# Optimization experiments

Hardware: AMD Instinct MI355X
Metric: run time of the kernel (lower is better)

Reference implementation:

```python
import jax, jax.numpy as jnp
import numpy as np

IMG = 640
STRIDES = (8, 16, 32)
A = 5            # anchors per level
NC = 80          # num classes
IOU_TH = 0.5
NEG_RATIO = 1.0


def make_priors():
    scales = [1.0, 1.5, 2.0, 2.5, 3.0]
    out = []
    for s in STRIDES:
        f = IMG // s
        ys, xs = np.meshgrid(np.arange(f), np.arange(f), indexing='ij')
        cx = ((xs + 0.5) / f).ravel()
        cy = ((ys + 0.5) / f).ravel()
        for sc in scales:  # anchor-major to match merge_features (A, h, w) order
            wh = min(sc * 4.0 * s / IMG, 1.0)
            out.append(np.stack([cx, cy, np.full_like(cx, wh), np.full_like(cx, wh)], 1))
    return np.concatenate(out, 0).astype(np.float32)  # [42000, 4] cxcywh


def merge_features(feats):
    outs = []
    for feat in feats:
        n, c, h, w = feat.shape
        f = feat.reshape(n, A, c // A, h, w).transpose(0, 1, 3, 4, 2)
        outs.append(f.reshape(n, A * h * w, c // A))
    return jnp.concatenate(outs, axis=1)  # [n, M, 85]


def box_iou_cxcywh(a, b):
    # a [T,4], b [M,4] (cx,cy,w,h) -> IoU [T,M]
    a1 = jnp.concatenate([a[:, :2] - a[:, 2:] / 2, a[:, :2] + a[:, 2:] / 2], -1)
    b1 = jnp.concatenate([b[:, :2] - b[:, 2:] / 2, b[:, :2] + b[:, 2:] / 2], -1)
    tl = jnp.maximum(a1[:, None, :2], b1[None, :, :2])
    br = jnp.minimum(a1[:, None, 2:], b1[None, :, 2:])
    wh = jnp.clip(br - tl, 0.0)
    inter = wh[..., 0] * wh[..., 1]
    area_a = a[:, 2] * a[:, 3]
    area_b = b[:, 2] * b[:, 3]
    return inter / (area_a[:, None] + area_b[None, :] - inter + 1e-9)


def build_targets(targets, priors, batch):
    ious = box_iou_cxcywh(targets[:, 2:6], priors)  # [Nt, M]
    Nt, M = ious.shape
    img_ids = targets[:, 0].astype(jnp.int32)

    def per_image(i):
        valid = img_ids == i  # [Nt]
        iv = jnp.where(valid[:, None], ious, -1.0)
        best_gt_overlap = iv.max(0)            # [M]
        best_gt_idx = iv.argmax(0)             # [M]
        best_prior_idx = iv.argmax(1)          # [Nt]
        # torch: index_fill_(1) then sequential best_gt_overlap[best_prior_idx[j]] = j
        local_j = (jnp.cumsum(valid.astype(jnp.int32)) - 1).astype(jnp.float32)
        scat_idx = jnp.where(valid, best_prior_idx, M)  # drop invalid rows
        best_gt_overlap = best_gt_overlap.at[scat_idx].set(local_j, mode='drop')
        bbox = targets[best_gt_idx, 2:6]
        clss = targets[best_gt_idx, 1] + 1.0
        clss = jnp.where(best_gt_overlap < IOU_TH, 0.0, clss)
        t_xy = (bbox[:, :2] - priors[:, :2]) / priors[:, 2:]
        t_wh = jnp.log(bbox[:, 2:] / priors[:, 2:])
        return t_xy, t_wh, clss

    return jax.vmap(per_image)(jnp.arange(batch))  # [B,M,2],[B,M,2],[B,M]


def _smooth_l1(x):
    ax = jnp.abs(x)
    return jnp.where(ax < 1.0, 0.5 * ax * ax, ax - 0.5)


def compute_loss(preds, priors, targets):
    n, m, _ = preds.shape
    t_xy, t_wh, t_cls = build_targets(targets, priors, n)
    pos = t_cls > 0
    posf = pos.astype(preds.dtype)
    num_pos = posf.sum()

    # lbox: smooth L1 on xy and wh over positives (mean over pos*2 elements each)
    den2 = jnp.maximum(num_pos * 2.0, 1.0)
    lbox = (_smooth_l1(preds[..., 0:2] - t_xy) * posf[..., None]).sum() / den2 \
         + (_smooth_l1(preds[..., 2:4] - t_wh) * posf[..., None]).sum() / den2

    # lcls: cross entropy over positives, labels = t_cls - 1
    labels = jnp.clip(t_cls.astype(jnp.int32) - 1, 0, NC - 1)
    logz = jax.nn.log_softmax(preds[..., 5:], axis=-1)
    ce = -jnp.take_along_axis(logz, labels[..., None], axis=-1)[..., 0]
    lcls = (ce * posf).sum() / jnp.maximum(num_pos, 1.0)

    # hard negative mining (no grad): double argsort rank trick
    obj = preds[..., 4]
    loss_c = jax.lax.stop_gradient(-jax.nn.log_sigmoid(obj))
    loss_c = jnp.where(pos, 0.0, loss_c)
    order = jnp.argsort(-loss_c, axis=-1)
    rank = jnp.argsort(order, axis=-1)
    num_neg = jnp.minimum(NEG_RATIO * num_pos, m - num_pos)
    neg = rank.astype(preds.dtype) < num_neg
    sel = (pos | neg).astype(preds.dtype)

    # lobj: BCE-with-logits over pos|neg
    z = posf
    bce = jnp.maximum(obj, 0.0) - obj * z + jnp.log1p(jnp.exp(-jnp.abs(obj)))
    lobj = (bce * sel).sum() / jnp.maximum(sel.sum(), 1.0)

    loss = lbox + lcls + lobj
    return jnp.stack([loss, lbox, lobj, lcls])


def setup_inputs() -> dict:
    key = jax.random.key(0)
    ks = jax.random.split(key, 6)
    feat0 = jax.random.normal(ks[0], (8, 425, 80, 80), jnp.float32)
    feat1 = jax.random.normal(ks[1], (8, 425, 40, 40), jnp.float32)
    feat2 = jax.random.normal(ks[2], (8, 425, 20, 20), jnp.float32)
    B, T = 8, 20
    img = jnp.repeat(jnp.arange(B, dtype=jnp.float32), T)
    cls = jax.random.randint(ks[3], (B * T,), 0, NC).astype(jnp.float32)
    cxcy = jax.random.uniform(ks[4], (B * T, 2), minval=0.2, maxval=0.8)
    wh = jax.random.uniform(ks[5], (B * T, 2), minval=0.05, maxval=0.3)
    targets = jnp.concatenate([img[:, None], cls[:, None], cxcy, wh], 1)
    priors = jnp.asarray(make_priors())
    return {"feat0": feat0, "feat1": feat1, "feat2": feat2,
            "targets": targets, "priors": priors}


def reference(feat0, feat1, feat2, targets, priors):
    preds = merge_features([feat0, feat1, feat2])  # [8, 42000, 85]
    return compute_loss(preds, priors, targets)    # [loss, lbox, lobj, lcls]
```

## Files before the change

### kernel.cpp

```cpp
#include <hip/hip_runtime.h>
#include <math.h>

#define MTOT 42000
#define NB 8
#define NCLS 80
#define CAP_LIST 4096
#define MAXT 256
#define NT_MAX 2048
#define GX_MAIN 165
#define NBLK_MAIN (GX_MAIN*NB)
#define NBLK_SEL 1313
#define NCH 32
#define CS 1313

#define O_OVR 0
#define O_GIX (O_OVR + NB*MTOT*4)
#define O_LSC (O_GIX + NB*MTOT*4)
#define O_BCE (O_LSC + NB*MTOT*4)
#define O_BPI (O_BCE + NB*MTOT*4)
#define O_LJ  (O_BPI + NT_MAX*4)
#define O_LST (O_LJ + NT_MAX*4)
#define O_BPP (O_LST + NB*MAXT*4)
#define O_PA  (O_BPP + NT_MAX*NCH*8)
#define O_PN  (O_PA + NBLK_MAIN*16)
#define O_P2  (O_PN + NBLK_MAIN*4)
#define O_BINL (O_P2 + NBLK_SEL*8)
#define O_HA  (O_BINL + NB*CAP_LIST*2*4)
#define O_HB  (O_HA + NB*256*4)
#define O_ACC (O_HB + NB*256*4)
#define O_ACCI (O_ACC + 64)
#define O_CNT (O_ACCI + 256)
#define O_ZEND (O_CNT + 64)

__device__ __forceinline__ float iou_cxcywh(float acx,float acy,float aw,float ah,
                                            float bcx,float bcy,float bw,float bh){
  float ax0=acx-aw*0.5f, ay0=acy-ah*0.5f, ax1=acx+aw*0.5f, ay1=acy+ah*0.5f;
  float bx0=bcx-bw*0.5f, by0=bcy-bh*0.5f, bx1=bcx+bw*0.5f, by1=bcy+bh*0.5f;
  float tlx=fmaxf(ax0,bx0), tly=fmaxf(ay0,by0);
  float brx=fminf(ax1,bx1), bry=fminf(ay1,by1);
  float wx=fmaxf(brx-tlx,0.f), wy=fmaxf(bry-tly,0.f);
  float inter=wx*wy;
  return inter/(aw*ah+bw*bh-inter+1e-9f);
}

__device__ __forceinline__ float sl1(float x){
  float ax=fabsf(x); return ax<1.f ? 0.5f*ax*ax : ax-0.5f;
}

__device__ __forceinline__ void feat_base(const float* f0,const float* f1,const float* f2,
                                          int i,int m,const float** basep,int* hwp){
  const float* fp; int hw, loc;
  if(m<32000){ fp=f0; hw=6400; loc=m; }
  else if(m<40000){ fp=f1; hw=1600; loc=m-32000; }
  else { fp=f2; hw=400; loc=m-40000; }
  int a=loc/hw, p=loc-a*hw;
  *basep = fp + (size_t)(i*425 + a*85)*(size_t)hw + p;
  *hwp = hw;
}

__global__ void k_prep(const float* __restrict__ tg, int nt, int* __restrict__ list,
                       int* __restrict__ cnt, int* __restrict__ lj){
  int t=blockIdx.x*blockDim.x+threadIdx.x;
  if(t>=nt) return;
  int img=(int)tg[t*6];
  int j=0;
  for(int q=0;q<t;q++) if((int)tg[q*6]==img) j++;
  lj[t]=j;
  if(img>=0 && img<NB){
    atomicAdd(&cnt[img],1);
    if(j<MAXT) list[img*MAXT+j]=t;
  }
}

__global__ void k_match(const float* __restrict__ tg, const float* __restrict__ priors,
                        const int* __restrict__ list, const int* __restrict__ cnt,
                        float* __restrict__ ovr, int* __restrict__ gix){
  __shared__ float st[MAXT*6];
  __shared__ int   sidx[MAXT];
  int i = blockIdx.y;
  int n = min(cnt[i],MAXT);
  for(int j=threadIdx.x;j<n;j+=blockDim.x){
    int t=list[i*MAXT+j];
    sidx[j]=t;
    #pragma unroll
    for(int q=0;q<6;q++) st[j*6+q]=tg[t*6+q];
  }
  __syncthreads();
  int m = blockIdx.x*blockDim.x + threadIdx.x;
  if(m>=MTOT) return;
  float4 pr = ((const float4*)priors)[m];
  float maxv=-1.0f; int bi=0;
  for(int j=0;j<n;j++){
    float v=iou_cxcywh(st[j*6+2],st[j*6+3],st[j*6+4],st[j*6+5], pr.x,pr.y,pr.z,pr.w);
    if(v>maxv){ maxv=v; bi=sidx[j]; }
  }
  ovr[i*MTOT+m]=maxv; gix[i*MTOT+m]=bi;
}

__global__ void k_bpA(const float* __restrict__ tg, const float* __restrict__ priors,
                      int nt, unsigned long long* __restrict__ part){
  __shared__ unsigned long long s[256];
  int t=blockIdx.y; if(t>=nt) return;
  int c=blockIdx.x;
  float acx=tg[t*6+2],acy=tg[t*6+3],aw=tg[t*6+4],ah=tg[t*6+5];
  int m0=c*CS, m1=min(m0+CS,MTOT);
  float bv=-1.f; int bm=0;
  for(int m=m0+threadIdx.x;m<m1;m+=blockDim.x){
    float4 pr=((const float4*)priors)[m];
    float v=iou_cxcywh(acx,acy,aw,ah,pr.x,pr.y,pr.z,pr.w);
    if(v>bv){ bv=v; bm=m; }
  }
  unsigned long long p = (bv<0.f) ? 0ull
      : (((unsigned long long)__float_as_uint(bv))<<32) | (unsigned)(~bm);
  s[threadIdx.x]=p;
  __syncthreads();
  for(int o=128;o>0;o>>=1){
    if(threadIdx.x<o){ if(s[threadIdx.x+o]>s[threadIdx.x]) s[threadIdx.x]=s[threadIdx.x+o]; }
    __syncthreads();
  }
  if(threadIdx.x==0) part[(size_t)t*NCH+c]=s[0];
}

__global__ void k_bpB(const unsigned long long* __restrict__ part, int nt,
                      int* __restrict__ bpi){
  __shared__ unsigned long long s[64];
  int t=blockIdx.x; if(t>=nt) return;
  int l=threadIdx.x;
  s[l]=(l<NCH)? part[(size_t)t*NCH+l] : 0ull;
  __syncthreads();
  for(int o=32;o>0;o>>=1){
    if(l<o){ if(s[l+o]>s[l]) s[l]=s[l+o]; }
    __syncthreads();
  }
  if(l==0) bpi[t]=~((unsigned)(s[0]&0xFFFFFFFFull));
}

__global__ void k_scatter(const float* __restrict__ tg, int nt,
                          const int* __restrict__ bpi, const int* __restrict__ lj,
                          float* __restrict__ ovr){
  int t=blockIdx.x*blockDim.x+threadIdx.x;
  if(t>=nt) return;
  int img=(int)tg[t*6];
  if(img<0||img>=NB) return;
  int myp=bpi[t];
  for(int q=t+1;q<nt;q++)
    if((int)tg[q*6]==img && bpi[q]==myp) return;
  ovr[img*MTOT+myp]=(float)lj[t];
}

__global__ void k_main(const float* __restrict__ f0,const float* __restrict__ f1,const float* __restrict__ f2,
                       const float* __restrict__ tg,const float* __restrict__ priors,
                       const float* __restrict__ ovr,const int* __restrict__ gix,
                       float* __restrict__ lsc,float* __restrict__ bcearr,
                       unsigned* __restrict__ histA,
                       float4* __restrict__ partA,int* __restrict__ partN){
  __shared__ unsigned h[256];
  __shared__ float sxy[4],swh[4],sbp[4],sce[4];
  __shared__ int snp[4];
  int tid=threadIdx.x;
  h[tid]=0;
  __syncthreads();
  int i=blockIdx.y;
  int m=blockIdx.x*blockDim.x+tid;
  int lane=tid&63, wid=tid>>6;
  bool valid=(m<MTOT);

  float lxy=0.f,lwh=0.f,bcep=0.f; int npos=0; bool pos=false; int gi=0;
  if(valid){
    int gid=i*MTOT+m;
    const float* base; int hw;
    feat_base(f0,f1,f2,i,m,&base,&hw);
    float ov=ovr[gid]; gi=gix[gid];
    float tc=tg[gi*6+1]+1.0f;
    pos=(ov>=0.5f)&&(tc>0.f);
    float obj=base[(size_t)4*hw];
    float sp=log1pf(expf(-fabsf(obj)));
    float bce=fmaxf(obj,0.f)-(pos?obj:0.f)+sp;
    float lc=pos?0.f:(fmaxf(-obj,0.f)+sp);
    lsc[gid]=lc; bcearr[gid]=bce;
    atomicAdd(&h[__float_as_uint(lc)>>24],1u);
    if(pos){
      npos=1; bcep=bce;
      float4 pr=((const float4*)priors)[m];
      float bx=tg[gi*6+2],by=tg[gi*6+3],bw=tg[gi*6+4],bh=tg[gi*6+5];
      float tx=(bx-pr.x)/pr.z, ty=(by-pr.y)/pr.w;
      float tw=logf(bw/pr.z), th=logf(bh/pr.w);
      lxy=sl1(base[0]-tx)+sl1(base[(size_t)hw]-ty);
      lwh=sl1(base[(size_t)2*hw]-tw)+sl1(base[(size_t)3*hw]-th);
    }
  }

  float wce=0.f;
  unsigned long long mask=__ballot(valid&&pos);
  while(mask){
    int s=__ffsll(mask)-1;
    mask&=mask-1;
    int m_s=__shfl(m,s);
    int gi_s=__shfl(gi,s);
    const float* bs; int hws;
    feat_base(f0,f1,f2,i,m_s,&bs,&hws);
    int label=(int)(tg[gi_s*6+1]+1.0f)-1;
    label=min(NCLS-1,max(0,label));
    float v0=bs[(size_t)(5+lane)*hws];
    float v1=(lane<16)?bs[(size_t)(69+lane)*hws]:-3.0e38f;
    float mx=fmaxf(v0,v1);
    #pragma unroll
    for(int o=32;o>0;o>>=1) mx=fmaxf(mx,__shfl_xor(mx,o));
    float se=expf(v0-mx)+((lane<16)?expf(v1-mx):0.f);
    float xl=((lane==label)?v0:0.f)+((lane<16&&lane+64==label)?v1:0.f);
    #pragma unroll
    for(int o=32;o>0;o>>=1){ se+=__shfl_xor(se,o); xl+=__shfl_xor(xl,o); }
    wce+=logf(se)+mx-xl;
  }

  #pragma unroll
  for(int o=32;o>0;o>>=1){
    lxy+=__shfl_xor(lxy,o); lwh+=__shfl_xor(lwh,o);
    bcep+=__shfl_xor(bcep,o); npos+=__shfl_xor(npos,o);
  }
  if(lane==0){ sxy[wid]=lxy; swh[wid]=lwh; sbp[wid]=bcep; sce[wid]=wce; snp[wid]=npos; }
  __syncthreads();
  unsigned c=h[tid];
  if(c) atomicAdd(&histA[i*256+tid],c);
  if(tid==0){
    float4 pa;
    pa.x=sxy[0]+sxy[1]+sxy[2]+sxy[3];
    pa.y=swh[0]+swh[1]+swh[2]+swh[3];
    pa.z=sce[0]+sce[1]+sce[2]+sce[3];
    pa.w=sbp[0]+sbp[1]+sbp[2]+sbp[3];
    int bid=blockIdx.y*gridDim.x+blockIdx.x;
    partA[bid]=pa;
    partN[bid]=snp[0]+snp[1]+snp[2]+snp[3];
  }
}

__global__ void k_red(const float4* __restrict__ partA,const int* __restrict__ partN,
                      float* __restrict__ accf,int* __restrict__ acci){
  __shared__ float a0[256],a1[256],a2[256],a3[256]; __shared__ int an[256];
  int t=threadIdx.x;
  float x=0,y=0,z=0,w=0; int n=0;
  for(int b=t;b<NBLK_MAIN;b+=256){
    float4 p=partA[b]; x+=p.x; y+=p.y; z+=p.z; w+=p.w; n+=partN[b];
  }
  a0[t]=x; a1[t]=y; a2[t]=z; a3[t]=w; an[t]=n;
  __syncthreads();
  for(int o=128;o>0;o>>=1){
    if(t<o){ a0[t]+=a0[t+o]; a1[t]+=a1[t+o]; a2[t]+=a2[t+o]; a3[t]+=a3[t+o]; an[t]+=an[t+o]; }
    __syncthreads();
  }
  if(t==0){ accf[0]=a0[0]; accf[1]=a1[0]; accf[2]=a2[0]; accf[3]=a3[0]; acci[0]=an[0]; }
}

__global__ void k_scanA(const unsigned* __restrict__ histA, int* __restrict__ acci){
  int i=blockIdx.x;
  __shared__ unsigned a[256];
  a[threadIdx.x]=histA[i*256+threadIdx.x];
  __syncthreads();
  if(threadIdx.x==0){
    int np=acci[0];
    int k=min(np, MTOT-np);
    if(k<=0){ acci[2+i]=0x7fffffff; acci[10+i]=0; return; }
    int run=0;
    for(int c=255;c>=0;c--){
      int cb=(int)a[c];
      if(run<k && run+cb>=k){ acci[2+i]=c; acci[10+i]=k-run; return; }
      run+=cb;
    }
    acci[2+i]=0; acci[10+i]=k-run;
  }
}

__global__ void k_histB(const float* __restrict__ lsc, const int* __restrict__ acci,
                        unsigned* __restrict__ histB){
  __shared__ unsigned h[256];
  h[threadIdx.x]=0;
  __syncthreads();
  int i=blockIdx.y;
  int ca=acci[2+i];
  int m=blockIdx.x*blockDim.x+threadIdx.x;
  if(m<MTOT && ca!=0x7fffffff){
    unsigned u=__float_as_uint(lsc[i*MTOT+m]);
    if((int)(u>>24)==ca) atomicAdd(&h[(u>>16)&0xFF],1u);
  }
  __syncthreads();
  unsigned c=h[threadIdx.x];
  if(c) atomicAdd(&histB[i*256+threadIdx.x],c);
}

__global__ void k_scanB(const unsigned* __restrict__ histB, int* __restrict__ acci){
  int i=blockIdx.x;
  __shared__ unsigned a[256];
  a[threadIdx.x]=histB[i*256+threadIdx.x];
  __syncthreads();
  if(threadIdx.x==0){
    int ca=acci[2+i], kres=acci[10+i];
    if(ca==0x7fffffff || kres<=0){ acci[2+i]=0x7fffffff; acci[10+i]=0; return; }
    int run=0;
    for(int f=255;f>=0;f--){
      int cb=(int)a[f];
      if(run<kres && run+cb>=kres){ acci[2+i]=(ca<<8)|f; acci[10+i]=kres-run; return; }
      run+=cb;
    }
    acci[2+i]=(ca<<8); acci[10+i]=kres-run;
  }
}

__global__ void k_select(const float* __restrict__ lsc,const float* __restrict__ bcearr,
                         int* __restrict__ acci,float2* __restrict__ part2,
                         int* __restrict__ binlist){
  __shared__ float ss[4]; __shared__ float sc[4];
  int tid=threadIdx.x, lane=tid&63, wid=tid>>6;
  int gid=blockIdx.x*blockDim.x+tid;
  float s=0.f, c=0.f;
  if(gid<NB*MTOT){
    int i=gid/MTOT;
    int bs_=acci[2+i];
    unsigned u=__float_as_uint(lsc[gid]);
    int bin=(int)(u>>16);
    if(bin>bs_){ s=bcearr[gid]; c=1.f; }
    else if(bin==bs_){
      int idx=atomicAdd(&acci[18+i],1);
      if(idx<CAP_LIST){
        binlist[((size_t)i*CAP_LIST+idx)*2  ]=(int)u;
        binlist[((size_t)i*CAP_LIST+idx)*2+1]=gid;
      }
    }
  }
  #pragma unroll
  for(int o=32;o>0;o>>=1){ s+=__shfl_xor(s,o); c+=__shfl_xor(c,o); }
  if(lane==0){ ss[wid]=s; sc[wid]=c; }
  __syncthreads();
  if(tid==0) part2[blockIdx.x]=make_float2(ss[0]+ss[1]+ss[2]+ss[3], sc[0]+sc[1]+sc[2]+sc[3]);
}

__global__ void k_ties(const float* __restrict__ bcearr,int* __restrict__ acci,
                       float* __restrict__ accf,const int* __restrict__ binlist){
  int i=blockIdx.x;
  if(acci[2+i]==0x7fffffff) return;
  int n=min(acci[18+i],CAP_LIST);
  int r=acci[10+i];
  for(int e=threadIdx.x;e<n;e+=blockDim.x){
    unsigned ue=(unsigned)binlist[((size_t)i*CAP_LIST+e)*2];
    int ge=binlist[((size_t)i*CAP_LIST+e)*2+1];
    int rank=0;
    for(int q=0;q<n;q++){
      unsigned uq=(unsigned)binlist[((size_t)i*CAP_LIST+q)*2];
      int gq=binlist[((size_t)i*CAP_LIST+q)*2+1];
      rank += ((uq>ue) || (uq==ue && gq<ge)) ? 1 : 0;
    }
    if(rank<r){
      atomicAdd(&accf[5], bcearr[ge]);
      atomicAdd(&acci[1], 1);
    }
  }
}

__global__ void k_final(const float* __restrict__ accf,const int* __restrict__ acci,
                        const float2* __restrict__ part2,float* __restrict__ out){
  __shared__ float ssum[256]; __shared__ float scnt[256];
  int t=threadIdx.x;
  float s=0.f,c=0.f;
  for(int b=t;b<NBLK_SEL;b+=256){ float2 p=part2[b]; s+=p.x; c+=p.y; }
  ssum[t]=s; scnt[t]=c;
  __syncthreads();
  for(int o=128;o>0;o>>=1){
    if(t<o){ ssum[t]+=ssum[t+o]; scnt[t]+=scnt[t+o]; }
    __syncthreads();
  }
  if(t==0){
    int np=acci[0];
    float npf=(float)np;
    float den2=fmaxf(2.f*npf,1.f);
    float lbox=accf[0]/den2 + accf[1]/den2;
    float lcls=accf[2]/fmaxf(npf,1.f);
    float negsum=ssum[0]+accf[5];
    float negcnt=scnt[0]+(float)acci[1];
    float selc=npf+negcnt;
    float lobj=(accf[3]+negsum)/fmaxf(selc,1.f);
    out[0]=lbox+lcls+lobj;
    out[1]=lbox;
    out[2]=lobj;
    out[3]=lcls;
  }
}

extern "C" void kernel_launch(void* const* d_in, const int* in_sizes, int n_in,
                              void* d_out, int out_size, void* d_ws, size_t ws_size,
                              hipStream_t stream) {
  const float* f0=(const float*)d_in[0];
  const float* f1=(const float*)d_in[1];
  const float* f2=(const float*)d_in[2];
  const float* tg=(const float*)d_in[3];
  const float* priors=(const float*)d_in[4];
  int nt = in_sizes[3]/6;
  if(nt>NT_MAX) nt=NT_MAX;

  char* ws=(char*)d_ws;
  float*    ovr    =(float*)   (ws+O_OVR);
  int*      gix    =(int*)     (ws+O_GIX);
  float*    lsc    =(float*)   (ws+O_LSC);
  float*    bcearr =(float*)   (ws+O_BCE);
  int*      bpi    =(int*)     (ws+O_BPI);
  int*      lj     =(int*)     (ws+O_LJ);
  int*      list   =(int*)     (ws+O_LST);
  unsigned long long* bpp=(unsigned long long*)(ws+O_BPP);
  float4*   partA  =(float4*)  (ws+O_PA);
  int*      partN  =(int*)     (ws+O_PN);
  float2*   part2  =(float2*)  (ws+O_P2);
  int*      binlist=(int*)     (ws+O_BINL);
  unsigned* histA  =(unsigned*)(ws+O_HA);
  unsigned* histB  =(unsigned*)(ws+O_HB);
  float*    accf   =(float*)   (ws+O_ACC);
  int*      acci   =(int*)     (ws+O_ACCI);
  int*      cnt    =(int*)     (ws+O_CNT);

  hipMemsetAsync(ws+O_HA, 0, (size_t)(O_ZEND-O_HA), stream);

  int ntb=(nt+255)/256;
  k_prep<<<ntb,256,0,stream>>>(tg,nt,list,cnt,lj);
  dim3 gm(GX_MAIN, NB);
  k_match<<<gm,256,0,stream>>>(tg,priors,list,cnt,ovr,gix);
  dim3 gbp(NCH, nt);
  k_bpA<<<gbp,256,0,stream>>>(tg,priors,nt,bpp);
  k_bpB<<<nt,64,0,stream>>>(bpp,nt,bpi);
  k_scatter<<<ntb,256,0,stream>>>(tg,nt,bpi,lj,ovr);
  k_main<<<gm,256,0,stream>>>(f0,f1,f2,tg,priors,ovr,gix,lsc,bcearr,histA,partA,partN);
  k_red<<<1,256,0,stream>>>(partA,partN,accf,acci);
  k_scanA<<<NB,256,0,stream>>>(histA,acci);
  k_histB<<<gm,256,0,stream>>>(lsc,acci,histB);
  k_scanB<<<NB,256,0,stream>>>(histB,acci);
  k_select<<<NBLK_SEL,256,0,stream>>>(lsc,bcearr,acci,part2,binlist);
  k_ties<<<NB,256,0,stream>>>(bcearr,acci,accf,binlist);
  k_final<<<1,256,0,stream>>>(accf,acci,part2,(float*)d_out);
}
```

Measured before the change: 158.9 us.

## Fuse all loss stages into one persistent kernel with grid barriers

```diff
diff --git a/kernel.cpp b/kernel.cpp
--- a/kernel.cpp
+++ b/kernel.cpp
@@ -7,30 +7,27 @@
 #define CAP_LIST 4096
 #define MAXT 256
 #define NT_MAX 2048
+#define NBLK 256
+#define KMAX 6
 #define GX_MAIN 165
-#define NBLK_MAIN (GX_MAIN*NB)
-#define NBLK_SEL 1313
 #define NCH 32
 #define CS 1313
 
 #define O_OVR 0
 #define O_GIX (O_OVR + NB*MTOT*4)
-#define O_LSC (O_GIX + NB*MTOT*4)
-#define O_BCE (O_LSC + NB*MTOT*4)
-#define O_BPI (O_BCE + NB*MTOT*4)
-#define O_LJ  (O_BPI + NT_MAX*4)
-#define O_LST (O_LJ + NT_MAX*4)
-#define O_BPP (O_LST + NB*MAXT*4)
+#define O_LST (O_GIX + NB*MTOT*4)
+#define O_LJ  (O_LST + NB*MAXT*4)
+#define O_CNT (O_LJ + NT_MAX*4)
+#define O_BPP (O_CNT + 64)
 #define O_PA  (O_BPP + NT_MAX*NCH*8)
-#define O_PN  (O_PA + NBLK_MAIN*16)
-#define O_P2  (O_PN + NBLK_MAIN*4)
-#define O_BINL (O_P2 + NBLK_SEL*8)
-#define O_HA  (O_BINL + NB*CAP_LIST*2*4)
+#define O_PN  (O_PA + NBLK*16)
+#define O_P2  (O_PN + NBLK*4)
+#define O_BINL (O_P2 + NBLK*8)
+#define O_ACC (O_BINL + NB*CAP_LIST*3*4)
+#define O_ACCI (O_ACC + 64)
+#define O_HA  (O_ACCI + 128)
 #define O_HB  (O_HA + NB*256*4)
-#define O_ACC (O_HB + NB*256*4)
-#define O_ACCI (O_ACC + 64)
-#define O_CNT (O_ACCI + 256)
-#define O_ZEND (O_CNT + 64)
+#define O_BAR (O_HB + NB*256*4)
 
 __device__ __forceinline__ float iou_cxcywh(float acx,float acy,float aw,float ah,
                                             float bcx,float bcy,float bw,float bh){
@@ -58,329 +55,382 @@
   *hwp = hw;
 }
 
-__global__ void k_prep(const float* __restrict__ tg, int nt, int* __restrict__ list,
-                       int* __restrict__ cnt, int* __restrict__ lj){
-  int t=blockIdx.x*blockDim.x+threadIdx.x;
-  if(t>=nt) return;
-  int img=(int)tg[t*6];
-  int j=0;
-  for(int q=0;q<t;q++) if((int)tg[q*6]==img) j++;
-  lj[t]=j;
-  if(img>=0 && img<NB){
-    atomicAdd(&cnt[img],1);
-    if(j<MAXT) list[img*MAXT+j]=t;
-  }
-}
-
-__global__ void k_match(const float* __restrict__ tg, const float* __restrict__ priors,
-                        const int* __restrict__ list, const int* __restrict__ cnt,
-                        float* __restrict__ ovr, int* __restrict__ gix){
-  __shared__ float st[MAXT*6];
-  __shared__ int   sidx[MAXT];
-  int i = blockIdx.y;
-  int n = min(cnt[i],MAXT);
-  for(int j=threadIdx.x;j<n;j+=blockDim.x){
-    int t=list[i*MAXT+j];
-    sidx[j]=t;
-    #pragma unroll
-    for(int q=0;q<6;q++) st[j*6+q]=tg[t*6+q];
-  }
-  __syncthreads();
-  int m = blockIdx.x*blockDim.x + threadIdx.x;
-  if(m>=MTOT) return;
-  float4 pr = ((const float4*)priors)[m];
-  float maxv=-1.0f; int bi=0;
-  for(int j=0;j<n;j++){
-    float v=iou_cxcywh(st[j*6+2],st[j*6+3],st[j*6+4],st[j*6+5], pr.x,pr.y,pr.z,pr.w);
-    if(v>maxv){ maxv=v; bi=sidx[j]; }
-  }
-  ovr[i*MTOT+m]=maxv; gix[i*MTOT+m]=bi;
-}
-
-__global__ void k_bpA(const float* __restrict__ tg, const float* __restrict__ priors,
-                      int nt, unsigned long long* __restrict__ part){
-  __shared__ unsigned long long s[256];
-  int t=blockIdx.y; if(t>=nt) return;
-  int c=blockIdx.x;
-  float acx=tg[t*6+2],acy=tg[t*6+3],aw=tg[t*6+4],ah=tg[t*6+5];
-  int m0=c*CS, m1=min(m0+CS,MTOT);
-  float bv=-1.f; int bm=0;
-  for(int m=m0+threadIdx.x;m<m1;m+=blockDim.x){
-    float4 pr=((const float4*)priors)[m];
-    float v=iou_cxcywh(acx,acy,aw,ah,pr.x,pr.y,pr.z,pr.w);
-    if(v>bv){ bv=v; bm=m; }
-  }
-  unsigned long long p = (bv<0.f) ? 0ull
-      : (((unsigned long long)__float_as_uint(bv))<<32) | (unsigned)(~bm);
-  s[threadIdx.x]=p;
-  __syncthreads();
-  for(int o=128;o>0;o>>=1){
-    if(threadIdx.x<o){ if(s[threadIdx.x+o]>s[threadIdx.x]) s[threadIdx.x]=s[threadIdx.x+o]; }
-    __syncthreads();
-  }
-  if(threadIdx.x==0) part[(size_t)t*NCH+c]=s[0];
-}
-
-__global__ void k_bpB(const unsigned long long* __restrict__ part, int nt,
-                      int* __restrict__ bpi){
-  __shared__ unsigned long long s[64];
-  int t=blockIdx.x; if(t>=nt) return;
-  int l=threadIdx.x;
-  s[l]=(l<NCH)? part[(size_t)t*NCH+l] : 0ull;
-  __syncthreads();
-  for(int o=32;o>0;o>>=1){
-    if(l<o){ if(s[l+o]>s[l]) s[l]=s[l+o]; }
-    __syncthreads();
-  }
-  if(l==0) bpi[t]=~((unsigned)(s[0]&0xFFFFFFFFull));
-}
-
-__global__ void k_scatter(const float* __restrict__ tg, int nt,
-                          const int* __restrict__ bpi, const int* __restrict__ lj,
-                          float* __restrict__ ovr){
-  int t=blockIdx.x*blockDim.x+threadIdx.x;
-  if(t>=nt) return;
-  int img=(int)tg[t*6];
-  if(img<0||img>=NB) return;
-  int myp=bpi[t];
-  for(int q=t+1;q<nt;q++)
-    if((int)tg[q*6]==img && bpi[q]==myp) return;
-  ovr[img*MTOT+myp]=(float)lj[t];
-}
-
-__global__ void k_main(const float* __restrict__ f0,const float* __restrict__ f1,const float* __restrict__ f2,
-                       const float* __restrict__ tg,const float* __restrict__ priors,
-                       const float* __restrict__ ovr,const int* __restrict__ gix,
-                       float* __restrict__ lsc,float* __restrict__ bcearr,
-                       unsigned* __restrict__ histA,
-                       float4* __restrict__ partA,int* __restrict__ partN){
-  __shared__ unsigned h[256];
-  __shared__ float sxy[4],swh[4],sbp[4],sce[4];
-  __shared__ int snp[4];
-  int tid=threadIdx.x;
-  h[tid]=0;
-  __syncthreads();
-  int i=blockIdx.y;
-  int m=blockIdx.x*blockDim.x+tid;
-  int lane=tid&63, wid=tid>>6;
-  bool valid=(m<MTOT);
-
-  float lxy=0.f,lwh=0.f,bcep=0.f; int npos=0; bool pos=false; int gi=0;
-  if(valid){
-    int gid=i*MTOT+m;
-    const float* base; int hw;
-    feat_base(f0,f1,f2,i,m,&base,&hw);
-    float ov=ovr[gid]; gi=gix[gid];
-    float tc=tg[gi*6+1]+1.0f;
-    pos=(ov>=0.5f)&&(tc>0.f);
-    float obj=base[(size_t)4*hw];
-    float sp=log1pf(expf(-fabsf(obj)));
-    float bce=fmaxf(obj,0.f)-(pos?obj:0.f)+sp;
-    float lc=pos?0.f:(fmaxf(-obj,0.f)+sp);
-    lsc[gid]=lc; bcearr[gid]=bce;
-    atomicAdd(&h[__float_as_uint(lc)>>24],1u);
-    if(pos){
-      npos=1; bcep=bce;
-      float4 pr=((const float4*)priors)[m];
-      float bx=tg[gi*6+2],by=tg[gi*6+3],bw=tg[gi*6+4],bh=tg[gi*6+5];
-      float tx=(bx-pr.x)/pr.z, ty=(by-pr.y)/pr.w;
-      float tw=logf(bw/pr.z), th=logf(bh/pr.w);
-      lxy=sl1(base[0]-tx)+sl1(base[(size_t)hw]-ty);
-      lwh=sl1(base[(size_t)2*hw]-tw)+sl1(base[(size_t)3*hw]-th);
-    }
-  }
-
-  float wce=0.f;
-  unsigned long long mask=__ballot(valid&&pos);
-  while(mask){
-    int s=__ffsll(mask)-1;
-    mask&=mask-1;
-    int m_s=__shfl(m,s);
-    int gi_s=__shfl(gi,s);
-    const float* bs; int hws;
-    feat_base(f0,f1,f2,i,m_s,&bs,&hws);
-    int label=(int)(tg[gi_s*6+1]+1.0f)-1;
-    label=min(NCLS-1,max(0,label));
-    float v0=bs[(size_t)(5+lane)*hws];
-    float v1=(lane<16)?bs[(size_t)(69+lane)*hws]:-3.0e38f;
-    float mx=fmaxf(v0,v1);
-    #pragma unroll
-    for(int o=32;o>0;o>>=1) mx=fmaxf(mx,__shfl_xor(mx,o));
-    float se=expf(v0-mx)+((lane<16)?expf(v1-mx):0.f);
-    float xl=((lane==label)?v0:0.f)+((lane<16&&lane+64==label)?v1:0.f);
-    #pragma unroll
-    for(int o=32;o>0;o>>=1){ se+=__shfl_xor(se,o); xl+=__shfl_xor(xl,o); }
-    wce+=logf(se)+mx-xl;
-  }
-
-  #pragma unroll
-  for(int o=32;o>0;o>>=1){
-    lxy+=__shfl_xor(lxy,o); lwh+=__shfl_xor(lwh,o);
-    bcep+=__shfl_xor(bcep,o); npos+=__shfl_xor(npos,o);
-  }
-  if(lane==0){ sxy[wid]=lxy; swh[wid]=lwh; sbp[wid]=bcep; sce[wid]=wce; snp[wid]=npos; }
-  __syncthreads();
-  unsigned c=h[tid];
-  if(c) atomicAdd(&histA[i*256+tid],c);
-  if(tid==0){
-    float4 pa;
-    pa.x=sxy[0]+sxy[1]+sxy[2]+sxy[3];
-    pa.y=swh[0]+swh[1]+swh[2]+swh[3];
-    pa.z=sce[0]+sce[1]+sce[2]+sce[3];
-    pa.w=sbp[0]+sbp[1]+sbp[2]+sbp[3];
-    int bid=blockIdx.y*gridDim.x+blockIdx.x;
-    partA[bid]=pa;
-    partN[bid]=snp[0]+snp[1]+snp[2]+snp[3];
-  }
-}
-
-__global__ void k_red(const float4* __restrict__ partA,const int* __restrict__ partN,
-                      float* __restrict__ accf,int* __restrict__ acci){
-  __shared__ float a0[256],a1[256],a2[256],a3[256]; __shared__ int an[256];
-  int t=threadIdx.x;
-  float x=0,y=0,z=0,w=0; int n=0;
-  for(int b=t;b<NBLK_MAIN;b+=256){
-    float4 p=partA[b]; x+=p.x; y+=p.y; z+=p.z; w+=p.w; n+=partN[b];
-  }
-  a0[t]=x; a1[t]=y; a2[t]=z; a3[t]=w; an[t]=n;
-  __syncthreads();
-  for(int o=128;o>0;o>>=1){
-    if(t<o){ a0[t]+=a0[t+o]; a1[t]+=a1[t+o]; a2[t]+=a2[t+o]; a3[t]+=a3[t+o]; an[t]+=an[t+o]; }
-    __syncthreads();
-  }
-  if(t==0){ accf[0]=a0[0]; accf[1]=a1[0]; accf[2]=a2[0]; accf[3]=a3[0]; acci[0]=an[0]; }
-}
-
-__global__ void k_scanA(const unsigned* __restrict__ histA, int* __restrict__ acci){
-  int i=blockIdx.x;
-  __shared__ unsigned a[256];
-  a[threadIdx.x]=histA[i*256+threadIdx.x];
+__device__ __forceinline__ void gbar(int* ctr){
   __syncthreads();
   if(threadIdx.x==0){
-    int np=acci[0];
-    int k=min(np, MTOT-np);
-    if(k<=0){ acci[2+i]=0x7fffffff; acci[10+i]=0; return; }
-    int run=0;
-    for(int c=255;c>=0;c--){
-      int cb=(int)a[c];
-      if(run<k && run+cb>=k){ acci[2+i]=c; acci[10+i]=k-run; return; }
-      run+=cb;
-    }
-    acci[2+i]=0; acci[10+i]=k-run;
-  }
-}
-
-__global__ void k_histB(const float* __restrict__ lsc, const int* __restrict__ acci,
-                        unsigned* __restrict__ histB){
+    __threadfence();
+    __hip_atomic_fetch_add(ctr,1,__ATOMIC_ACQ_REL,__HIP_MEMORY_SCOPE_AGENT);
+    while(__hip_atomic_load(ctr,__ATOMIC_ACQUIRE,__HIP_MEMORY_SCOPE_AGENT)<NBLK)
+      __builtin_amdgcn_s_sleep(4);
+    __threadfence();
+  }
+  __syncthreads();
+}
+
+__global__ void k_init0(int* bars){
+  if(threadIdx.x<8) bars[threadIdx.x]=0;
+}
+
+__device__ __forceinline__ void fine_scan(const unsigned* hb,int ca,int kres,int* bs_out,int* r_out){
+  if(ca==0x7fffffff){ *bs_out=0x7fffffff; *r_out=0; return; }
+  int run=0, bs=-1, r=0;
+  for(int f=255;f>=0;f--){
+    int cb=(int)hb[f];
+    if(run<kres && run+cb>=kres){ bs=(ca<<8)|f; r=kres-run; break; }
+    run+=cb;
+  }
+  if(bs<0){ bs=(ca<<8); r=kres-run; }
+  *bs_out=bs; *r_out=r;
+}
+
+__global__ void __launch_bounds__(256,1) k_mega(
+    const float* __restrict__ f0,const float* __restrict__ f1,const float* __restrict__ f2,
+    const float* __restrict__ tg,const float* __restrict__ priors,
+    int nt, char* __restrict__ ws, float* __restrict__ out)
+{
+  float* ovr=(float*)(ws+O_OVR);
+  int* gix=(int*)(ws+O_GIX);
+  int* list=(int*)(ws+O_LST);
+  int* lj=(int*)(ws+O_LJ);
+  int* cnt=(int*)(ws+O_CNT);
+  unsigned long long* bpp=(unsigned long long*)(ws+O_BPP);
+  float4* partA=(float4*)(ws+O_PA);
+  int* partN=(int*)(ws+O_PN);
+  float2* part2=(float2*)(ws+O_P2);
+  int* binlist=(int*)(ws+O_BINL);
+  float* accf=(float*)(ws+O_ACC);
+  int* acci=(int*)(ws+O_ACCI);
+  unsigned* histA=(unsigned*)(ws+O_HA);
+  unsigned* histB=(unsigned*)(ws+O_HB);
+  int* bars=(int*)(ws+O_BAR);
+
+  int b=blockIdx.x, tid=threadIdx.x;
+  int lane=tid&63, wid=tid>>6;
+  int i_img=b>>5, cb0=b&31;
+
+  __shared__ __align__(16) float st[MAXT*6];
+  __shared__ int sidx[MAXT];
+  __shared__ unsigned long long su[256];
   __shared__ unsigned h[256];
-  h[threadIdx.x]=0;
-  __syncthreads();
-  int i=blockIdx.y;
-  int ca=acci[2+i];
-  int m=blockIdx.x*blockDim.x+threadIdx.x;
-  if(m<MTOT && ca!=0x7fffffff){
-    unsigned u=__float_as_uint(lsc[i*MTOT+m]);
-    if((int)(u>>24)==ca) atomicAdd(&h[(u>>16)&0xFF],1u);
-  }
-  __syncthreads();
-  unsigned c=h[threadIdx.x];
-  if(c) atomicAdd(&histB[i*256+threadIdx.x],c);
-}
-
-__global__ void k_scanB(const unsigned* __restrict__ histB, int* __restrict__ acci){
-  int i=blockIdx.x;
-  __shared__ unsigned a[256];
-  a[threadIdx.x]=histB[i*256+threadIdx.x];
-  __syncthreads();
-  if(threadIdx.x==0){
-    int ca=acci[2+i], kres=acci[10+i];
-    if(ca==0x7fffffff || kres<=0){ acci[2+i]=0x7fffffff; acci[10+i]=0; return; }
-    int run=0;
-    for(int f=255;f>=0;f--){
-      int cb=(int)a[f];
-      if(run<kres && run+cb>=kres){ acci[2+i]=(ca<<8)|f; acci[10+i]=kres-run; return; }
-      run+=cb;
-    }
-    acci[2+i]=(ca<<8); acci[10+i]=kres-run;
-  }
-}
-
-__global__ void k_select(const float* __restrict__ lsc,const float* __restrict__ bcearr,
-                         int* __restrict__ acci,float2* __restrict__ part2,
-                         int* __restrict__ binlist){
-  __shared__ float ss[4]; __shared__ float sc[4];
-  int tid=threadIdx.x, lane=tid&63, wid=tid>>6;
-  int gid=blockIdx.x*blockDim.x+tid;
-  float s=0.f, c=0.f;
-  if(gid<NB*MTOT){
-    int i=gid/MTOT;
-    int bs_=acci[2+i];
-    unsigned u=__float_as_uint(lsc[gid]);
-    int bin=(int)(u>>16);
-    if(bin>bs_){ s=bcearr[gid]; c=1.f; }
-    else if(bin==bs_){
-      int idx=atomicAdd(&acci[18+i],1);
-      if(idx<CAP_LIST){
-        binlist[((size_t)i*CAP_LIST+idx)*2  ]=(int)u;
-        binlist[((size_t)i*CAP_LIST+idx)*2+1]=gid;
-      }
-    }
-  }
-  #pragma unroll
-  for(int o=32;o>0;o>>=1){ s+=__shfl_xor(s,o); c+=__shfl_xor(c,o); }
-  if(lane==0){ ss[wid]=s; sc[wid]=c; }
-  __syncthreads();
-  if(tid==0) part2[blockIdx.x]=make_float2(ss[0]+ss[1]+ss[2]+ss[3], sc[0]+sc[1]+sc[2]+sc[3]);
-}
-
-__global__ void k_ties(const float* __restrict__ bcearr,int* __restrict__ acci,
-                       float* __restrict__ accf,const int* __restrict__ binlist){
-  int i=blockIdx.x;
-  if(acci[2+i]==0x7fffffff) return;
-  int n=min(acci[18+i],CAP_LIST);
-  int r=acci[10+i];
-  for(int e=threadIdx.x;e<n;e+=blockDim.x){
-    unsigned ue=(unsigned)binlist[((size_t)i*CAP_LIST+e)*2];
-    int ge=binlist[((size_t)i*CAP_LIST+e)*2+1];
-    int rank=0;
-    for(int q=0;q<n;q++){
-      unsigned uq=(unsigned)binlist[((size_t)i*CAP_LIST+q)*2];
-      int gq=binlist[((size_t)i*CAP_LIST+q)*2+1];
-      rank += ((uq>ue) || (uq==ue && gq<ge)) ? 1 : 0;
-    }
-    if(rank<r){
-      atomicAdd(&accf[5], bcearr[ge]);
-      atomicAdd(&acci[1], 1);
-    }
-  }
-}
-
-__global__ void k_final(const float* __restrict__ accf,const int* __restrict__ acci,
-                        const float2* __restrict__ part2,float* __restrict__ out){
-  __shared__ float ssum[256]; __shared__ float scnt[256];
-  int t=threadIdx.x;
-  float s=0.f,c=0.f;
-  for(int b=t;b<NBLK_SEL;b+=256){ float2 p=part2[b]; s+=p.x; c+=p.y; }
-  ssum[t]=s; scnt[t]=c;
-  __syncthreads();
-  for(int o=128;o>0;o>>=1){
-    if(t<o){ ssum[t]+=ssum[t+o]; scnt[t]+=scnt[t+o]; }
-    __syncthreads();
-  }
-  if(t==0){
-    int np=acci[0];
-    float npf=(float)np;
-    float den2=fmaxf(2.f*npf,1.f);
-    float lbox=accf[0]/den2 + accf[1]/den2;
-    float lcls=accf[2]/fmaxf(npf,1.f);
-    float negsum=ssum[0]+accf[5];
-    float negcnt=scnt[0]+(float)acci[1];
-    float selc=npf+negcnt;
-    float lobj=(accf[3]+negsum)/fmaxf(selc,1.f);
-    out[0]=lbox+lcls+lobj;
-    out[1]=lbox;
-    out[2]=lobj;
-    out[3]=lcls;
+  __shared__ int tbp[NT_MAX];
+  __shared__ int timg[NT_MAX];
+  __shared__ float rA[4],rB[4],rC[4],rD[4];
+  __shared__ int rN[4];
+
+  {
+    int g=b*256+tid;
+    if(g<NB*256) histA[g]=0u;
+    else if(g<2*NB*256) histB[g-NB*256]=0u;
+    else if(g<2*NB*256+NB) acci[18+(g-2*NB*256)]=0;
+    if(g<nt){
+      int img=(int)tg[g*6];
+      int j=0;
+      for(int q=0;q<g;q++) if((int)tg[q*6]==img) j++;
+      lj[g]=j;
+      if(img>=0&&img<NB&&j<MAXT) list[img*MAXT+j]=g;
+    }
+    if(g>=NBLK*256-NB){
+      int im=g-(NBLK*256-NB);
+      int c=0;
+      for(int q=0;q<nt;q++) if((int)tg[q*6]==im) c++;
+      cnt[im]=c;
+    }
+  }
+  gbar(&bars[0]);
+
+  {
+    int n=min(max(cnt[i_img],0),MAXT);
+    for(int j=tid;j<n;j+=256){
+      int t=list[i_img*MAXT+j];
+      t=min(max(t,0),nt-1);
+      sidx[j]=t;
+      #pragma unroll
+      for(int q=0;q<6;q++) st[j*6+q]=tg[t*6+q];
+    }
+    __syncthreads();
+    for(int k=0;k<KMAX;k++){
+      int cb=cb0+32*k;
+      if(cb>=GX_MAIN) break;
+      int m=cb*256+tid;
+      if(m<MTOT){
+        float4 pr=((const float4*)priors)[m];
+        float maxv=-1.f; int bi=0;
+        for(int j=0;j<n;j++){
+          float v=iou_cxcywh(st[j*6+2],st[j*6+3],st[j*6+4],st[j*6+5],pr.x,pr.y,pr.z,pr.w);
+          if(v>maxv){ maxv=v; bi=sidx[j]; }
+        }
+        ovr[i_img*MTOT+m]=maxv; gix[i_img*MTOT+m]=bi;
+      }
+    }
+    __syncthreads();
+    int nvb=nt*NCH;
+    int niter=(nvb+NBLK-1)/NBLK;
+    for(int q=0;q<niter;q++){
+      int vb=b+NBLK*q;
+      bool act=(vb<nvb);
+      unsigned long long p=0ull;
+      if(act){
+        int t=vb/NCH, c=vb-(vb/NCH)*NCH;
+        float acx=tg[t*6+2],acy=tg[t*6+3],aw=tg[t*6+4],ah=tg[t*6+5];
+        int m0=c*CS, m1=min(m0+CS,MTOT);
+        float bv=-1.f; int bm=0;
+        for(int m=m0+tid;m<m1;m+=256){
+          float4 pr=((const float4*)priors)[m];
+          float v=iou_cxcywh(acx,acy,aw,ah,pr.x,pr.y,pr.z,pr.w);
+          if(v>bv){ bv=v; bm=m; }
+        }
+        p=(bv<0.f)?0ull:(((unsigned long long)__float_as_uint(bv))<<32)|(unsigned)(~bm);
+      }
+      su[tid]=p;
+      __syncthreads();
+      for(int o=128;o>0;o>>=1){
+        if(tid<o){ if(su[tid+o]>su[tid]) su[tid]=su[tid+o]; }
+        __syncthreads();
+      }
+      if(act&&tid==0){ int t=vb/NCH, c=vb-(vb/NCH)*NCH; bpp[(size_t)t*NCH+c]=su[0]; }
+      __syncthreads();
+    }
+  }
+  gbar(&bars[1]);
+
+  if(b==0){
+    for(int t=tid;t<nt;t+=256){
+      unsigned long long best=0ull;
+      const unsigned long long* pp=&bpp[(size_t)t*NCH];
+      for(int c=0;c<NCH;c++){ unsigned long long v=pp[c]; if(v>best) best=v; }
+      int bm=~((unsigned)(best&0xFFFFFFFFull));
+      tbp[t]=min(max(bm,0),MTOT-1);
+      timg[t]=(int)tg[t*6];
+    }
+    __syncthreads();
+    for(int t=tid;t<nt;t+=256){
+      int img=timg[t];
+      if(img<0||img>=NB) continue;
+      int myp=tbp[t];
+      bool last=true;
+      for(int q=t+1;q<nt;q++) if(timg[q]==img&&tbp[q]==myp){ last=false; break; }
+      if(last) ovr[img*MTOT+myp]=(float)lj[t];
+    }
+  }
+  gbar(&bars[2]);
+
+  float lcv[KMAX], bcev[KMAX];
+  unsigned validb=0;
+  {
+    float lxy=0.f,lwh=0.f,bcep=0.f,wce=0.f; int npos=0;
+    h[tid]=0u;
+    __syncthreads();
+    #pragma unroll
+    for(int k=0;k<KMAX;k++){
+      int cb=cb0+32*k;
+      int m=cb*256+tid;
+      bool valid=(cb<GX_MAIN)&&(m<MTOT);
+      float lc=0.f,bce=0.f; bool pos=false; int gi=0;
+      if(valid){
+        int gid=i_img*MTOT+m;
+        const float* base; int hw;
+        feat_base(f0,f1,f2,i_img,m,&base,&hw);
+        float ov=ovr[gid];
+        gi=min(max(gix[gid],0),nt-1);
+        float tc=tg[gi*6+1]+1.f;
+        pos=(ov>=0.5f)&&(tc>0.f);
+        float obj=base[(size_t)4*hw];
+        float sp=log1pf(expf(-fabsf(obj)));
+        bce=fmaxf(obj,0.f)-(pos?obj:0.f)+sp;
+        lc=pos?0.f:(fmaxf(-obj,0.f)+sp);
+        atomicAdd(&h[__float_as_uint(lc)>>24],1u);
+        if(pos){
+          npos++; bcep+=bce;
+          float4 pr=((const float4*)priors)[m];
+          float bx=tg[gi*6+2],by=tg[gi*6+3],bw=tg[gi*6+4],bh=tg[gi*6+5];
+          float tx=(bx-pr.x)/pr.z, ty=(by-pr.y)/pr.w;
+          float tw=logf(bw/pr.z), th=logf(bh/pr.w);
+          lxy+=sl1(base[0]-tx)+sl1(base[(size_t)hw]-ty);
+          lwh+=sl1(base[(size_t)2*hw]-tw)+sl1(base[(size_t)3*hw]-th);
+        }
+      }
+      lcv[k]=lc; bcev[k]=bce;
+      validb|=(valid?1u:0u)<<k;
+      int m_cur=m;
+      unsigned long long mask=__ballot(valid&&pos);
+      while(mask){
+        int s=__ffsll((unsigned long long)mask)-1;
+        mask&=mask-1;
+        int m_s=__shfl(m_cur,s);
+        int gi_s=__shfl(gi,s);
+        const float* bs2; int hws;
+        feat_base(f0,f1,f2,i_img,m_s,&bs2,&hws);
+        int label=(int)(tg[gi_s*6+1]+1.f)-1;
+        label=min(NCLS-1,max(0,label));
+        float v0=bs2[(size_t)(5+lane)*hws];
+        float v1=(lane<16)?bs2[(size_t)(69+lane)*hws]:-3.0e38f;
+        float mx=fmaxf(v0,v1);
+        #pragma unroll
+        for(int o=32;o>0;o>>=1) mx=fmaxf(mx,__shfl_xor(mx,o));
+        float se=expf(v0-mx)+((lane<16)?expf(v1-mx):0.f);
+        float xl=((lane==label)?v0:0.f)+((lane<16&&lane+64==label)?v1:0.f);
+        #pragma unroll
+        for(int o=32;o>0;o>>=1){ se+=__shfl_xor(se,o); xl+=__shfl_xor(xl,o); }
+        wce+=logf(se)+mx-xl;
+      }
+    }
+    #pragma unroll
+    for(int o=32;o>0;o>>=1){
+      lxy+=__shfl_xor(lxy,o); lwh+=__shfl_xor(lwh,o);
+      bcep+=__shfl_xor(bcep,o); npos+=__shfl_xor(npos,o);
+    }
+    if(lane==0){ rA[wid]=lxy; rB[wid]=lwh; rC[wid]=wce; rD[wid]=bcep; rN[wid]=npos; }
+    __syncthreads();
+    unsigned hc=h[tid];
+    if(hc) atomicAdd(&histA[i_img*256+tid],hc);
+    if(tid==0){
+      partA[b]=make_float4(rA[0]+rA[1]+rA[2]+rA[3], rB[0]+rB[1]+rB[2]+rB[3],
+                           rC[0]+rC[1]+rC[2]+rC[3], rD[0]+rD[1]+rD[2]+rD[3]);
+      partN[b]=rN[0]+rN[1]+rN[2]+rN[3];
+    }
+  }
+  gbar(&bars[3]);
+
+  if(b<NB){
+    int* an=(int*)sidx;
+    an[tid]=partN[tid];
+    __syncthreads();
+    for(int o=128;o>0;o>>=1){ if(tid<o) an[tid]+=an[tid+o]; __syncthreads(); }
+    int np=an[0];
+    if(b==0){
+      float4* fr=(float4*)st;
+      fr[tid]=partA[tid];
+      __syncthreads();
+      for(int o=128;o>0;o>>=1){
+        if(tid<o){
+          fr[tid].x+=fr[tid+o].x; fr[tid].y+=fr[tid+o].y;
+          fr[tid].z+=fr[tid+o].z; fr[tid].w+=fr[tid+o].w;
+        }
+        __syncthreads();
+      }
+      if(tid==0){ accf[0]=fr[0].x; accf[1]=fr[0].y; accf[2]=fr[0].z; accf[3]=fr[0].w; acci[0]=np; }
+    }
+    h[tid]=histA[b*256+tid];
+    __syncthreads();
+    if(tid==0){
+      int kk=min(np,MTOT-np);
+      if(kk<=0){ acci[2+b]=0x7fffffff; acci[10+b]=0; }
+      else{
+        int run=0, ca=-1, kres=0;
+        for(int c2=255;c2>=0;c2--){
+          int cbn=(int)h[c2];
+          if(run<kk&&run+cbn>=kk){ ca=c2; kres=kk-run; break; }
+          run+=cbn;
+        }
+        if(ca<0){ ca=0; kres=kk-run; }
+        acci[2+b]=ca; acci[10+b]=kres;
+      }
+    }
+  }
+  gbar(&bars[4]);
+
+  {
+    int ca=acci[2+i_img];
+    if(ca!=0x7fffffff){
+      #pragma unroll
+      for(int k=0;k<KMAX;k++){
+        if(validb&(1u<<k)){
+          unsigned u=__float_as_uint(lcv[k]);
+          if((int)(u>>24)==ca) atomicAdd(&histB[i_img*256+((u>>16)&0xFF)],1u);
+        }
+      }
+    }
+  }
+  gbar(&bars[5]);
+
+  if(b<NB){
+    int ca=acci[2+b], kres=acci[10+b];
+    h[tid]=(ca==0x7fffffff)?0u:histB[b*256+tid];
+    __syncthreads();
+    if(tid==0){
+      int bs,r; fine_scan(h,ca,kres,&bs,&r);
+      acci[2+b]=bs; acci[10+b]=r;
+    }
+  }
+  gbar(&bars[6]);
+
+  {
+    int bs_=acci[2+i_img];
+    float s=0.f,c=0.f;
+    #pragma unroll
+    for(int k=0;k<KMAX;k++){
+      if(validb&(1u<<k)){
+        unsigned u=__float_as_uint(lcv[k]);
+        int bin=(int)(u>>16);
+        if(bin>bs_){ s+=bcev[k]; c+=1.f; }
+        else if(bin==bs_){
+          int idx=atomicAdd(&acci[18+i_img],1);
+          if(idx<CAP_LIST){
+            int gid=i_img*MTOT+(cb0+32*k)*256+tid;
+            binlist[((size_t)i_img*CAP_LIST+idx)*3  ]=(int)u;
+            binlist[((size_t)i_img*CAP_LIST+idx)*3+1]=gid;
+            binlist[((size_t)i_img*CAP_LIST+idx)*3+2]=__float_as_int(bcev[k]);
+          }
+        }
+      }
+    }
+    #pragma unroll
+    for(int o=32;o>0;o>>=1){ s+=__shfl_xor(s,o); c+=__shfl_xor(c,o); }
+    if(lane==0){ rA[wid]=s; rB[wid]=c; }
+    __syncthreads();
+    if(tid==0) part2[b]=make_float2(rA[0]+rA[1]+rA[2]+rA[3], rB[0]+rB[1]+rB[2]+rB[3]);
+  }
+  gbar(&bars[7]);
+
+  if(b==0){
+    float* fs=st; float* fc=st+256;
+    float2 p2=part2[tid];
+    fs[tid]=p2.x; fc[tid]=p2.y;
+    __syncthreads();
+    for(int o=128;o>0;o>>=1){
+      if(tid<o){ fs[tid]+=fs[tid+o]; fc[tid]+=fc[tid+o]; }
+      __syncthreads();
+    }
+    float negsum=fs[0], negcnt=fc[0];
+    __syncthreads();
+    float tsum=0.f; int tcnt=0;
+    for(int i=0;i<NB;i++){
+      int bs=acci[2+i];
+      if(bs==0x7fffffff) continue;
+      int n=min(acci[18+i],CAP_LIST);
+      int r=acci[10+i];
+      for(int e=tid;e<n;e+=256){
+        const int* be=&binlist[((size_t)i*CAP_LIST+e)*3];
+        unsigned ue=(unsigned)be[0]; int ge=be[1];
+        int rank=0;
+        for(int q=0;q<n;q++){
+          const int* bq=&binlist[((size_t)i*CAP_LIST+q)*3];
+          unsigned uq=(unsigned)bq[0]; int gq=bq[1];
+          rank += ((uq>ue)||(uq==ue&&gq<ge))?1:0;
+        }
+        if(rank<r){ tsum+=__int_as_float(be[2]); tcnt++; }
+      }
+    }
+    float ftc=(float)tcnt;
+    #pragma unroll
+    for(int o=32;o>0;o>>=1){ tsum+=__shfl_xor(tsum,o); ftc+=__shfl_xor(ftc,o); }
+    if(lane==0){ rA[wid]=tsum; rB[wid]=ftc; }
+    __syncthreads();
+    if(tid==0){
+      negsum+=rA[0]+rA[1]+rA[2]+rA[3];
+      negcnt+=rB[0]+rB[1]+rB[2]+rB[3];
+      int np=acci[0];
+      float npf=(float)np;
+      float den2=fmaxf(2.f*npf,1.f);
+      float lbox=accf[0]/den2+accf[1]/den2;
+      float lcls=accf[2]/fmaxf(npf,1.f);
+      float selc=npf+negcnt;
+      float lobj=(accf[3]+negsum)/fmaxf(selc,1.f);
+      out[0]=lbox+lcls+lobj;
+      out[1]=lbox;
+      out[2]=lobj;
+      out[3]=lcls;
+    }
   }
 }
 
@@ -394,42 +444,11 @@
   const float* priors=(const float*)d_in[4];
   int nt = in_sizes[3]/6;
   if(nt>NT_MAX) nt=NT_MAX;
+  if(nt<1) nt=1;
 
   char* ws=(char*)d_ws;
-  float*    ovr    =(float*)   (ws+O_OVR);
-  int*      gix    =(int*)     (ws+O_GIX);
-  float*    lsc    =(float*)   (ws+O_LSC);
-  float*    bcearr =(float*)   (ws+O_BCE);
-  int*      bpi    =(int*)     (ws+O_BPI);
-  int*      lj     =(int*)     (ws+O_LJ);
-  int*      list   =(int*)     (ws+O_LST);
-  unsigned long long* bpp=(unsigned long long*)(ws+O_BPP);
-  float4*   partA  =(float4*)  (ws+O_PA);
-  int*      partN  =(int*)     (ws+O_PN);
-  float2*   part2  =(float2*)  (ws+O_P2);
-  int*      binlist=(int*)     (ws+O_BINL);
-  unsigned* histA  =(unsigned*)(ws+O_HA);
-  unsigned* histB  =(unsigned*)(ws+O_HB);
-  float*    accf   =(float*)   (ws+O_ACC);
-  int*      acci   =(int*)     (ws+O_ACCI);
-  int*      cnt    =(int*)     (ws+O_CNT);
-
-  hipMemsetAsync(ws+O_HA, 0, (size_t)(O_ZEND-O_HA), stream);
-
-  int ntb=(nt+255)/256;
-  k_prep<<<ntb,256,0,stream>>>(tg,nt,list,cnt,lj);
-  dim3 gm(GX_MAIN, NB);
-  k_match<<<gm,256,0,stream>>>(tg,priors,list,cnt,ovr,gix);
-  dim3 gbp(NCH, nt);
-  k_bpA<<<gbp,256,0,stream>>>(tg,priors,nt,bpp);
-  k_bpB<<<nt,64,0,stream>>>(bpp,nt,bpi);
-  k_scatter<<<ntb,256,0,stream>>>(tg,nt,bpi,lj,ovr);
-  k_main<<<gm,256,0,stream>>>(f0,f1,f2,tg,priors,ovr,gix,lsc,bcearr,histA,partA,partN);
-  k_red<<<1,256,0,stream>>>(partA,partN,accf,acci);
-  k_scanA<<<NB,256,0,stream>>>(histA,acci);
-  k_histB<<<gm,256,0,stream>>>(lsc,acci,histB);
-  k_scanB<<<NB,256,0,stream>>>(histB,acci);
-  k_select<<<NBLK_SEL,256,0,stream>>>(lsc,bcearr,acci,part2,binlist);
-  k_ties<<<NB,256,0,stream>>>(bcearr,acci,accf,binlist);
-  k_final<<<1,256,0,stream>>>(accf,acci,part2,(float*)d_out);
-}
+  int* bars=(int*)(ws+O_BAR);
+
+  k_init0<<<1,64,0,stream>>>(bars);
+  k_mega<<<NBLK,256,0,stream>>>(f0,f1,f2,tg,priors,nt,ws,(float*)d_out);
+}
```

New measurement: 499.6 us. 214% more time.
